# Kernel tuning notes

Measured on AMD Instinct MI355X. Metric: run time of the kernel, lower is better.

Reference implementation:

```python
import jax, jax.numpy as jnp
import numpy as np

B, TQ, TK = 4, 128, 512
DQ = DK = DV = H = 1024


def setup_inputs() -> dict:
    key = jax.random.key(0)
    ks = jax.random.split(key, 7)
    s = 0.05  # keep tanh out of saturation
    return {
        "query": jax.random.normal(ks[0], (B, TQ, DQ), dtype=jnp.float32),
        "key": jax.random.normal(ks[1], (B, TK, DK), dtype=jnp.float32),
        "value": jax.random.normal(ks[2], (B, TK, DV), dtype=jnp.float32),
        "Wq": jax.random.normal(ks[3], (DQ, H), dtype=jnp.float32) * s,
        "bq": jax.random.normal(ks[4], (H,), dtype=jnp.float32) * s,
        "Wk": jax.random.normal(ks[5], (DK, H), dtype=jnp.float32) * s,
        "v": jax.random.normal(ks[6], (H,), dtype=jnp.float32) * s,
    }


def reference(query, key, value, Wq, bq, Wk, v):
    # additive (Bahdanau) attention
    wq = jnp.einsum("bqd,dh->bqh", query, Wq) + bq      # [B,Tq,H]
    uh = jnp.einsum("bkd,dh->bkh", key, Wk)             # [B,Tk,H]
    # broadcast add -> [B,Tq,Tk,H], tanh, project to scalar score
    scores = jnp.einsum("bqkh,h->bqk",
                        jnp.tanh(wq[:, :, None, :] + uh[:, None, :, :]), v)
    attn = jax.nn.softmax(scores, axis=-1)              # [B,Tq,Tk]
    h = jnp.einsum("bqk,bkv->bqv", attn, value)         # [B,Tq,Dv]
    return h, attn
```

## Files before the change

kernel.cpp:

```cpp
#include <hip/hip_runtime.h>
#include <hip/hip_bf16.h>

typedef float f32x4 __attribute__((ext_vector_type(4)));
typedef float f32x2 __attribute__((ext_vector_type(2)));
typedef short s16x8 __attribute__((ext_vector_type(8)));
typedef short s16x4 __attribute__((ext_vector_type(4)));

#define NB  4
#define NTQ 128
#define NTK 512
#define NH  1024
#define ECLAMP 3.0e4f

__device__ __forceinline__ unsigned short f2bf(float x) {
    unsigned u = __builtin_bit_cast(unsigned, x);
    u += 0x7FFFu + ((u >> 16) & 1u);
    return (unsigned short)(u >> 16);
}

#define K2E  2.8853900817779268f

#define GLD16(gp, lp) __builtin_amdgcn_global_load_lds( \
    (const __attribute__((address_space(1))) unsigned int*)(gp), \
    (__attribute__((address_space(3))) unsigned int*)(lp), 16, 0, 0)

__global__ __launch_bounds__(256) void prep_kernel(
    const float* __restrict__ Q, const float* __restrict__ K,
    const float* __restrict__ Wq, const float* __restrict__ Wk,
    const float* __restrict__ value,
    short* __restrict__ Qb, short* __restrict__ Kb,
    short* __restrict__ WqT, short* __restrict__ WkT, short* __restrict__ valT)
{
    const int t = threadIdx.x, bx = blockIdx.x;
    if (bx < 640) {
        const float* src; short* dst; size_t base;
        if (bx < 128) { src = Q; dst = Qb; base = (size_t)bx * 4096; }
        else          { src = K; dst = Kb; base = (size_t)(bx - 128) * 4096; }
        #pragma unroll
        for (int i = 0; i < 4; ++i) {
            const size_t off = base + (size_t)(i * 256 + t) * 4;
            const float4 vv = *(const float4*)(src + off);
            s16x4 o = { (short)f2bf(vv.x), (short)f2bf(vv.y),
                        (short)f2bf(vv.z), (short)f2bf(vv.w) };
            *(s16x4*)(dst + off) = o;
        }
        return;
    }
    __shared__ float tile[64][65];
    const int i = bx - 640;
    const float* src; short* dst; int Cs, Rs, r0, c0;
    if (i < 256)      { src = Wq; dst = WqT; Cs = 1024; Rs = 1024; r0 = (i >> 4) * 64; c0 = (i & 15) * 64; }
    else if (i < 512) { const int j = i - 256; src = Wk; dst = WkT; Cs = 1024; Rs = 1024; r0 = (j >> 4) * 64; c0 = (j & 15) * 64; }
    else {
        const int j = i - 512, b = j >> 7, ti = j & 127;
        src = value + (size_t)b * 512 * 1024; dst = valT + (size_t)b * 1024 * 512;
        Cs = 1024; Rs = 512; r0 = (ti >> 4) * 64; c0 = (ti & 15) * 64;
    }
    {
        const int c = (t & 15) * 4;
        #pragma unroll
        for (int it = 0; it < 4; ++it) {
            const int r = (t >> 4) + it * 16;
            const float4 vv = *(const float4*)(src + (size_t)(r0 + r) * Cs + c0 + c);
            tile[r][c + 0] = vv.x; tile[r][c + 1] = vv.y;
            tile[r][c + 2] = vv.z; tile[r][c + 3] = vv.w;
        }
    }
    __syncthreads();
    {
        const int r = (t & 15) * 4;
        #pragma unroll
        for (int it = 0; it < 4; ++it) {
            const int c = (t >> 4) + it * 16;
            s16x4 o = { (short)f2bf(tile[r + 0][c]), (short)f2bf(tile[r + 1][c]),
                        (short)f2bf(tile[r + 2][c]), (short)f2bf(tile[r + 3][c]) };
            *(s16x4*)(dst + (size_t)(c0 + c) * Rs + r0 + r) = o;
        }
    }
}

__global__ __launch_bounds__(256) void mm_kernel(
    const short* __restrict__ Qb, const short* __restrict__ Kb,
    const short* __restrict__ WqT, const short* __restrict__ WkT,
    const float* __restrict__ bq,
    float* __restrict__ Ea_out, unsigned short* __restrict__ EbT)
{
    __shared__ short ldsA[2][128][64];
    __shared__ short ldsB[2][64][64];
    const int t = threadIdx.x;
    const int bx0 = blockIdx.x;
    const int bx = (bx0 & 7) * 40 + (bx0 >> 3);
    const bool g1 = bx < 64;
    const short *A, *B; int m0, n0;
    if (g1) { A = Qb; B = WqT; m0 = (bx >> 4) * 128; n0 = (bx & 15) * 64; }
    else    { const int i = bx - 64; A = Kb; B = WkT; m0 = (i >> 4) * 128; n0 = (i & 15) * 64; }
    A += (size_t)m0 * 1024; B += (size_t)n0 * 1024;

    f32x4 acc[4][2];
    #pragma unroll
    for (int i = 0; i < 4; ++i)
        #pragma unroll
        for (int j = 0; j < 2; ++j) acc[i][j] = f32x4{0.f, 0.f, 0.f, 0.f};

    const int lane = t & 63, wid = t >> 6;
    const int wr = wid >> 1, wc = wid & 1;
    const int fr = lane & 15, fko = (lane >> 4) * 16;

    #define STAGE_MM(buf, k0) do {                                              \
        _Pragma("unroll")                                                       \
        for (int it = 0; it < 4; ++it) {                                        \
            const int idx = it * 256 + t;                                       \
            const int row = idx >> 3, c16 = idx & 7;                            \
            const int sc = c16 ^ (row & 7);                                     \
            GLD16(A + (size_t)row * 1024 + (k0) + sc * 8,                       \
                  &ldsA[buf][0][0] + idx * 8);                                  \
        }                                                                       \
        _Pragma("unroll")                                                       \
        for (int it = 0; it < 2; ++it) {                                        \
            const int idx = it * 256 + t;                                       \
            const int row = idx >> 3, c16 = idx & 7;                            \
            const int sc = c16 ^ (row & 7);                                     \
            GLD16(B + (size_t)row * 1024 + (k0) + sc * 8,                       \
                  &ldsB[buf][0][0] + idx * 8);                                  \
        }                                                                       \
    } while (0)

    #define COMPUTE_MM(buf) do {                                                \
        _Pragma("unroll")                                                       \
        for (int kk = 0; kk < 2; ++kk) {                                        \
            s16x8 af[4], bfv[2];                                                \
            _Pragma("unroll")                                                   \
            for (int i = 0; i < 4; ++i) {                                       \
                const int rowA = wr * 64 + i * 16 + fr;                         \
                int offA = rowA * 128 + kk * 64 + fko; offA ^= (rowA & 7) << 4; \
                af[i] = *(const s16x8*)((const char*)&ldsA[buf][0][0] + offA);  \
            }                                                                   \
            _Pragma("unroll")                                                   \
            for (int ni = 0; ni < 2; ++ni) {                                    \
                const int rowB = wc * 32 + ni * 16 + fr;                        \
                int offB = rowB * 128 + kk * 64 + fko; offB ^= (rowB & 7) << 4; \
                bfv[ni] = *(const s16x8*)((const char*)&ldsB[buf][0][0] + offB);\
            }                                                                   \
            _Pragma("unroll")                                                   \
            for (int mi = 0; mi < 4; ++mi)                                      \
                _Pragma("unroll")                                               \
                for (int ni = 0; ni < 2; ++ni)                                  \
                    acc[mi][ni] = __builtin_amdgcn_mfma_f32_16x16x32_bf16(      \
                                      af[mi], bfv[ni], acc[mi][ni], 0, 0, 0);   \
        }                                                                       \
    } while (0)

    STAGE_MM(0, 0);
    __syncthreads();
    int cur = 0;
    for (int s = 0; s < 15; ++s) {
        STAGE_MM(cur ^ 1, (s + 1) * 64);
        COMPUTE_MM(cur);
        __syncthreads();
        cur ^= 1;
    }
    COMPUTE_MM(cur);

    const int row0 = (lane >> 4) * 4;
    if (g1) {
        #pragma unroll
        for (int ni = 0; ni < 2; ++ni) {
            const int n = n0 + wc * 32 + ni * 16 + fr;
            const float bias = bq[n];
            #pragma unroll
            for (int mi = 0; mi < 4; ++mi) {
                const int m = m0 + wr * 64 + mi * 16 + row0;
                #pragma unroll
                for (int j = 0; j < 4; ++j)
                    Ea_out[(size_t)(m + j) * 1024 + n] =
                        fminf(__builtin_amdgcn_exp2f(K2E * (acc[mi][ni][j] + bias)), ECLAMP);
            }
        }
    } else {
        #pragma unroll
        for (int mi = 0; mi < 4; ++mi) {
            const int m = m0 + wr * 64 + mi * 16 + row0;
            const int b = m >> 9, kk = m & 511;
            #pragma unroll
            for (int ni = 0; ni < 2; ++ni) {
                const int n = n0 + wc * 32 + ni * 16 + fr;
                s16x4 ev;
                #pragma unroll
                for (int j = 0; j < 4; ++j)
                    ev[j] = (short)f2bf(fminf(__builtin_amdgcn_exp2f(K2E * acc[mi][ni][j]), ECLAMP));
                *(s16x4*)&EbT[((size_t)b * 1024 + n) * 512 + kk] = ev;
            }
        }
    }
    #undef STAGE_MM
    #undef COMPUTE_MM
}

__global__ __launch_bounds__(1024, 4) void scores_softmax(
    const unsigned short* __restrict__ EbT, const float* __restrict__ Ea,
    const float* __restrict__ v,
    float* __restrict__ attn_out, short* __restrict__ attnb)
{
    __shared__ float4 s_eav[1024];
    __shared__ float  s_part[8][2][512];
    __shared__ float  s_red[16];
    const int t = threadIdx.x, bx = blockIdx.x;
    const int b = bx & 3;
    const int q2 = bx >> 2;
    const int bq0 = b * 128 + q2 * 2;
    const int kq = t & 127;
    const int hs = t >> 7;
    const int lane = t & 63, wid = t >> 6;

    s_eav[t] = make_float4(Ea[(size_t)(bq0 + 0) * 1024 + t],
                           Ea[(size_t)(bq0 + 1) * 1024 + t],
                           v[t], 0.f);
    __syncthreads();

    const int h0 = hs * 128;
    const uint2* up = (const uint2*)(EbT + ((size_t)(b * 1024 + h0)) * 512) + kq;
    f32x2 a0lo = {0.f, 0.f}, a0hi = {0.f, 0.f};
    f32x2 a1lo = {0.f, 0.f}, a1hi = {0.f, 0.f};
    const f32x2 one2 = {1.f, 1.f};

    #pragma unroll 2
    for (int hg = 0; hg < 32; ++hg) {
        const int hb = hg * 4;
        const uint2 r0 = up[(size_t)(hb + 0) * 128];
        const uint2 r1 = up[(size_t)(hb + 1) * 128];
        const uint2 r2 = up[(size_t)(hb + 2) * 128];
        const uint2 r3 = up[(size_t)(hb + 3) * 128];
        const float4 ev0 = s_eav[h0 + hb + 0];
        const float4 ev1 = s_eav[h0 + hb + 1];
        const float4 ev2 = s_eav[h0 + hb + 2];
        const float4 ev3 = s_eav[h0 + hb + 3];
        #define UNPK(r) f32x2{__builtin_bit_cast(float, (r) << 16),            \
                              __builtin_bit_cast(float, (r) & 0xFFFF0000u)}
        const f32x2 b0lo = UNPK(r0.x), b0hi = UNPK(r0.y);
        const f32x2 b1lo = UNPK(r1.x), b1hi = UNPK(r1.y);
        const f32x2 b2lo = UNPK(r2.x), b2hi = UNPK(r2.y);
        const f32x2 b3lo = UNPK(r3.x), b3hi = UNPK(r3.y);
        #undef UNPK
        const f32x2 vv0 = {ev0.z, ev0.z}, vv1 = {ev1.z, ev1.z};
        const f32x2 vv2 = {ev2.z, ev2.z}, vv3 = {ev3.z, ev3.z};

        #define GRPPK(accv, EA0, EA1, EA2, EA3, B0, B1, B2, B3) do {            \
            const f32x2 u0 = B0 * EA0 + one2;                                   \
            const f32x2 u1 = B1 * EA1 + one2;                                   \
            const f32x2 u2 = B2 * EA2 + one2;                                   \
            const f32x2 u3 = B3 * EA3 + one2;                                   \
            const f32x2 d01 = u0 * u1, d23 = u2 * u3;                           \
            f32x2 n01 = vv0 * u1; n01 = vv1 * u0 + n01;                         \
            f32x2 n23 = vv2 * u3; n23 = vv3 * u2 + n23;                         \
            f32x2 n = n01 * d23; n = n23 * d01 + n;                             \
            const f32x2 den = d01 * d23;                                        \
            const f32x2 r = {__builtin_amdgcn_rcpf(den.x),                      \
                             __builtin_amdgcn_rcpf(den.y)};                     \
            accv = n * r + accv;                                                \
        } while (0)

        {
            const f32x2 e0 = {ev0.x, ev0.x}, e1 = {ev1.x, ev1.x};
            const f32x2 e2 = {ev2.x, ev2.x}, e3 = {ev3.x, ev3.x};
            GRPPK(a0lo, e0, e1, e2, e3, b0lo, b1lo, b2lo, b3lo);
            GRPPK(a0hi, e0, e1, e2, e3, b0hi, b1hi, b2hi, b3hi);
        }
        {
            const f32x2 e0 = {ev0.y, ev0.y}, e1 = {ev1.y, ev1.y};
            const f32x2 e2 = {ev2.y, ev2.y}, e3 = {ev3.y, ev3.y};
            GRPPK(a1lo, e0, e1, e2, e3, b0lo, b1lo, b2lo, b3lo);
            GRPPK(a1hi, e0, e1, e2, e3, b0hi, b1hi, b2hi, b3hi);
        }
        #undef GRPPK
    }
    *(f32x4*)&s_part[hs][0][kq * 4] = f32x4{a0lo.x, a0lo.y, a0hi.x, a0hi.y};
    *(f32x4*)&s_part[hs][1][kq * 4] = f32x4{a1lo.x, a1lo.y, a1hi.x, a1hi.y};
    __syncthreads();

    const int kk = t & 511, qq = t >> 9;
    float z = 0.f;
    #pragma unroll
    for (int j = 0; j < 8; ++j) z += s_part[j][qq][kk];
    z *= -2.0f;

    float m = z;
    #pragma unroll
    for (int off = 32; off > 0; off >>= 1)
        m = fmaxf(m, __shfl_xor(m, off, 64));
    if (lane == 0) s_red[wid] = m;
    __syncthreads();
    float mx = s_red[qq * 8];
    #pragma unroll
    for (int w = 1; w < 8; ++w) mx = fmaxf(mx, s_red[qq * 8 + w]);
    const float p = __expf(z - mx);
    __syncthreads();

    float sl = p;
    #pragma unroll
    for (int off = 32; off > 0; off >>= 1)
        sl += __shfl_xor(sl, off, 64);
    if (lane == 0) s_red[wid] = sl;
    __syncthreads();
    float s = 0.f;
    #pragma unroll
    for (int w = 0; w < 8; ++w) s += s_red[qq * 8 + w];

    const float a = p * (1.0f / s);
    attn_out[(size_t)(bq0 + qq) * 512 + kk] = a;
    attnb[(size_t)(bq0 + qq) * 512 + kk] = (short)f2bf(a);
}

__global__ __launch_bounds__(256) void pv_gemm(
    const short* __restrict__ attnb, const short* __restrict__ valT,
    float* __restrict__ outh)
{
    __shared__ short ldsA[2][128][64];
    __shared__ short ldsB[2][64][64];
    const int t = threadIdx.x, bx = blockIdx.x;
    const int b = bx >> 4, nt = bx & 15;
    const int n0 = nt * 64;
    const short* A = attnb + (size_t)b * 128 * 512;
    const short* B = valT + (size_t)b * 1024 * 512 + (size_t)n0 * 512;

    f32x4 acc[4][2];
    #pragma unroll
    for (int i = 0; i < 4; ++i)
        #pragma unroll
        for (int j = 0; j < 2; ++j) acc[i][j] = f32x4{0.f, 0.f, 0.f, 0.f};

    const int lane = t & 63, wid = t >> 6;
    const int wr = wid >> 1, wc = wid & 1;
    const int fr = lane & 15, fko = (lane >> 4) * 16;

    #define STAGE_PV(buf, k0) do {                                              \
        _Pragma("unroll")                                                       \
        for (int it = 0; it < 4; ++it) {                                        \
            const int idx = it * 256 + t;                                       \
            const int row = idx >> 3, c16 = idx & 7;                            \
            const int sc = c16 ^ (row & 7);                                     \
            GLD16(A + (size_t)row * 512 + (k0) + sc * 8,                        \
                  &ldsA[buf][0][0] + idx * 8);                                  \
        }                                                                       \
        _Pragma("unroll")                                                       \
        for (int it = 0; it < 2; ++it) {                                        \
            const int idx = it * 256 + t;                                       \
            const int row = idx >> 3, c16 = idx & 7;                            \
            const int sc = c16 ^ (row & 7);                                     \
            GLD16(B + (size_t)row * 512 + (k0) + sc * 8,                        \
                  &ldsB[buf][0][0] + idx * 8);                                  \
        }                                                                       \
    } while (0)

    #define COMPUTE_PV(buf) do {                                                \
        _Pragma("unroll")                                                       \
        for (int kk = 0; kk < 2; ++kk) {                                        \
            s16x8 af[4], bfv[2];                                                \
            _Pragma("unroll")                                                   \
            for (int i = 0; i < 4; ++i) {                                       \
                const int rowA = wr * 64 + i * 16 + fr;                         \
                int offA = rowA * 128 + kk * 64 + fko; offA ^= (rowA & 7) << 4; \
                af[i] = *(const s16x8*)((const char*)&ldsA[buf][0][0] + offA);  \
            }                                                                   \
            _Pragma("unroll")                                                   \
            for (int ni = 0; ni < 2; ++ni) {                                    \
                const int rowB = wc * 32 + ni * 16 + fr;                        \
                int offB = rowB * 128 + kk * 64 + fko; offB ^= (rowB & 7) << 4; \
                bfv[ni] = *(const s16x8*)((const char*)&ldsB[buf][0][0] + offB);\
            }                                                                   \
            _Pragma("unroll")                                                   \
            for (int mi = 0; mi < 4; ++mi)                                      \
                _Pragma("unroll")                                               \
                for (int ni = 0; ni < 2; ++ni)                                  \
                    acc[mi][ni] = __builtin_amdgcn_mfma_f32_16x16x32_bf16(      \
                                      af[mi], bfv[ni], acc[mi][ni], 0, 0, 0);   \
        }                                                                       \
    } while (0)

    STAGE_PV(0, 0);
    __syncthreads();
    int cur = 0;
    for (int s = 0; s < 7; ++s) {
        STAGE_PV(cur ^ 1, (s + 1) * 64);
        COMPUTE_PV(cur);
        __syncthreads();
        cur ^= 1;
    }
    COMPUTE_PV(cur);

    const int row0 = (lane >> 4) * 4;
    #pragma unroll
    for (int ni = 0; ni < 2; ++ni) {
        const int n = n0 + wc * 32 + ni * 16 + fr;
        #pragma unroll
        for (int mi = 0; mi < 4; ++mi) {
            const int m = wr * 64 + mi * 16 + row0;
            #pragma unroll
            for (int j = 0; j < 4; ++j)
                outh[(size_t)(b * 128 + m + j) * 1024 + n] = acc[mi][ni][j];
        }
    }
    #undef STAGE_PV
    #undef COMPUTE_PV
}

extern "C" void kernel_launch(void* const* d_in, const int* in_sizes, int n_in,
                              void* d_out, int out_size, void* d_ws, size_t ws_size,
                              hipStream_t stream)
{
    const float* query = (const float*)d_in[0];
    const float* key   = (const float*)d_in[1];
    const float* value = (const float*)d_in[2];
    const float* Wq    = (const float*)d_in[3];
    const float* bq    = (const float*)d_in[4];
    const float* Wk    = (const float*)d_in[5];
    const float* v     = (const float*)d_in[6];
    float* out = (float*)d_out;

    char* w = (char*)d_ws;
    float*          ws_Ea  = (float*)w;
    unsigned short* ws_EbT = (unsigned short*)(w + (2u << 20));
    short* Qb     = (short*)(w + (6u << 20));
    short* Kb     = (short*)(w + (7u << 20));
    short* WqT    = (short*)(w + (11u << 20));
    short* WkT    = (short*)(w + (13u << 20));
    short* valT   = (short*)(w + (15u << 20));
    short* attnb  = (short*)(w + (19u << 20));

    float* out_h    = out;
    float* out_attn = out + (size_t)NB * NTQ * NH;

    prep_kernel   <<<dim3(1664), dim3(256),  0, stream>>>(query, key, Wq, Wk, value,
                                                          Qb, Kb, WqT, WkT, valT);
    mm_kernel     <<<dim3(320),  dim3(256),  0, stream>>>(Qb, Kb, WqT, WkT, bq, ws_Ea, ws_EbT);
    scores_softmax<<<dim3(256),  dim3(1024), 0, stream>>>(ws_EbT, ws_Ea, v, out_attn, attnb);
    pv_gemm       <<<dim3(64),   dim3(256),  0, stream>>>(attnb, valT, out_h);
}
```

Before: 66.32 us.

## Process one query per scores_softmax block and double the grid size

```diff
diff --git a/kernel.cpp b/kernel.cpp
--- a/kernel.cpp
+++ b/kernel.cpp
@@ -196,31 +196,28 @@
     #undef COMPUTE_MM
 }
 
-__global__ __launch_bounds__(1024, 4) void scores_softmax(
+__global__ __launch_bounds__(1024, 8) void scores_softmax(
     const unsigned short* __restrict__ EbT, const float* __restrict__ Ea,
     const float* __restrict__ v,
     float* __restrict__ attn_out, short* __restrict__ attnb)
 {
-    __shared__ float4 s_eav[1024];
-    __shared__ float  s_part[8][2][512];
+    __shared__ float2 s_eav[1024];
+    __shared__ float  s_part[8][512];
     __shared__ float  s_red[16];
     const int t = threadIdx.x, bx = blockIdx.x;
     const int b = bx & 3;
-    const int q2 = bx >> 2;
-    const int bq0 = b * 128 + q2 * 2;
+    const int q = bx >> 2;
+    const int bq = b * 128 + q;
     const int kq = t & 127;
     const int hs = t >> 7;
     const int lane = t & 63, wid = t >> 6;
 
-    s_eav[t] = make_float4(Ea[(size_t)(bq0 + 0) * 1024 + t],
-                           Ea[(size_t)(bq0 + 1) * 1024 + t],
-                           v[t], 0.f);
+    s_eav[t] = make_float2(Ea[(size_t)bq * 1024 + t], v[t]);
     __syncthreads();
 
     const int h0 = hs * 128;
     const uint2* up = (const uint2*)(EbT + ((size_t)(b * 1024 + h0)) * 512) + kq;
-    f32x2 a0lo = {0.f, 0.f}, a0hi = {0.f, 0.f};
-    f32x2 a1lo = {0.f, 0.f}, a1hi = {0.f, 0.f};
+    f32x2 alo = {0.f, 0.f}, ahi = {0.f, 0.f};
     const f32x2 one2 = {1.f, 1.f};
 
     #pragma unroll 2
@@ -230,10 +227,10 @@
         const uint2 r1 = up[(size_t)(hb + 1) * 128];
         const uint2 r2 = up[(size_t)(hb + 2) * 128];
         const uint2 r3 = up[(size_t)(hb + 3) * 128];
-        const float4 ev0 = s_eav[h0 + hb + 0];
-        const float4 ev1 = s_eav[h0 + hb + 1];
-        const float4 ev2 = s_eav[h0 + hb + 2];
-        const float4 ev3 = s_eav[h0 + hb + 3];
+        const float2 ev0 = s_eav[h0 + hb + 0];
+        const float2 ev1 = s_eav[h0 + hb + 1];
+        const float2 ev2 = s_eav[h0 + hb + 2];
+        const float2 ev3 = s_eav[h0 + hb + 3];
         #define UNPK(r) f32x2{__builtin_bit_cast(float, (r) << 16),            \
                               __builtin_bit_cast(float, (r) & 0xFFFF0000u)}
         const f32x2 b0lo = UNPK(r0.x), b0hi = UNPK(r0.y);
@@ -241,14 +238,16 @@
         const f32x2 b2lo = UNPK(r2.x), b2hi = UNPK(r2.y);
         const f32x2 b3lo = UNPK(r3.x), b3hi = UNPK(r3.y);
         #undef UNPK
-        const f32x2 vv0 = {ev0.z, ev0.z}, vv1 = {ev1.z, ev1.z};
-        const f32x2 vv2 = {ev2.z, ev2.z}, vv3 = {ev3.z, ev3.z};
-
-        #define GRPPK(accv, EA0, EA1, EA2, EA3, B0, B1, B2, B3) do {            \
-            const f32x2 u0 = B0 * EA0 + one2;                                   \
-            const f32x2 u1 = B1 * EA1 + one2;                                   \
-            const f32x2 u2 = B2 * EA2 + one2;                                   \
-            const f32x2 u3 = B3 * EA3 + one2;                                   \
+        const f32x2 e0 = {ev0.x, ev0.x}, e1 = {ev1.x, ev1.x};
+        const f32x2 e2 = {ev2.x, ev2.x}, e3 = {ev3.x, ev3.x};
+        const f32x2 vv0 = {ev0.y, ev0.y}, vv1 = {ev1.y, ev1.y};
+        const f32x2 vv2 = {ev2.y, ev2.y}, vv3 = {ev3.y, ev3.y};
+
+        #define GRPPK(accv, B0, B1, B2, B3) do {                                \
+            const f32x2 u0 = B0 * e0 + one2;                                    \
+            const f32x2 u1 = B1 * e1 + one2;                                    \
+            const f32x2 u2 = B2 * e2 + one2;                                    \
+            const f32x2 u3 = B3 * e3 + one2;                                    \
             const f32x2 d01 = u0 * u1, d23 = u2 * u3;                           \
             f32x2 n01 = vv0 * u1; n01 = vv1 * u0 + n01;                         \
             f32x2 n23 = vv2 * u3; n23 = vv3 * u2 + n23;                         \
@@ -259,28 +258,17 @@
             accv = n * r + accv;                                                \
         } while (0)
 
-        {
-            const f32x2 e0 = {ev0.x, ev0.x}, e1 = {ev1.x, ev1.x};
-            const f32x2 e2 = {ev2.x, ev2.x}, e3 = {ev3.x, ev3.x};
-            GRPPK(a0lo, e0, e1, e2, e3, b0lo, b1lo, b2lo, b3lo);
-            GRPPK(a0hi, e0, e1, e2, e3, b0hi, b1hi, b2hi, b3hi);
-        }
-        {
-            const f32x2 e0 = {ev0.y, ev0.y}, e1 = {ev1.y, ev1.y};
-            const f32x2 e2 = {ev2.y, ev2.y}, e3 = {ev3.y, ev3.y};
-            GRPPK(a1lo, e0, e1, e2, e3, b0lo, b1lo, b2lo, b3lo);
-            GRPPK(a1hi, e0, e1, e2, e3, b0hi, b1hi, b2hi, b3hi);
-        }
+        GRPPK(alo, b0lo, b1lo, b2lo, b3lo);
+        GRPPK(ahi, b0hi, b1hi, b2hi, b3hi);
         #undef GRPPK
     }
-    *(f32x4*)&s_part[hs][0][kq * 4] = f32x4{a0lo.x, a0lo.y, a0hi.x, a0hi.y};
-    *(f32x4*)&s_part[hs][1][kq * 4] = f32x4{a1lo.x, a1lo.y, a1hi.x, a1hi.y};
-    __syncthreads();
-
-    const int kk = t & 511, qq = t >> 9;
+    *(f32x4*)&s_part[hs][kq * 4] = f32x4{alo.x, alo.y, ahi.x, ahi.y};
+    __syncthreads();
+
+    const int kk = t & 511;
     float z = 0.f;
     #pragma unroll
-    for (int j = 0; j < 8; ++j) z += s_part[j][qq][kk];
+    for (int j = 0; j < 8; ++j) z += s_part[j][kk];
     z *= -2.0f;
 
     float m = z;
@@ -289,9 +277,9 @@
         m = fmaxf(m, __shfl_xor(m, off, 64));
     if (lane == 0) s_red[wid] = m;
     __syncthreads();
-    float mx = s_red[qq * 8];
-    #pragma unroll
-    for (int w = 1; w < 8; ++w) mx = fmaxf(mx, s_red[qq * 8 + w]);
+    float mx = s_red[0];
+    #pragma unroll
+    for (int w = 1; w < 8; ++w) mx = fmaxf(mx, s_red[w]);
     const float p = __expf(z - mx);
     __syncthreads();
 
@@ -303,11 +291,13 @@
     __syncthreads();
     float s = 0.f;
     #pragma unroll
-    for (int w = 0; w < 8; ++w) s += s_red[qq * 8 + w];
-
-    const float a = p * (1.0f / s);
-    attn_out[(size_t)(bq0 + qq) * 512 + kk] = a;
-    attnb[(size_t)(bq0 + qq) * 512 + kk] = (short)f2bf(a);
+    for (int w = 0; w < 8; ++w) s += s_red[w];
+
+    if (t < 512) {
+        const float a = p * (1.0f / s);
+        attn_out[(size_t)bq * 512 + kk] = a;
+        attnb[(size_t)bq * 512 + kk] = (short)f2bf(a);
+    }
 }
 
 __global__ __launch_bounds__(256) void pv_gemm(
@@ -432,6 +422,6 @@
     prep_kernel   <<<dim3(1664), dim3(256),  0, stream>>>(query, key, Wq, Wk, value,
                                                           Qb, Kb, WqT, WkT, valT);
     mm_kernel     <<<dim3(320),  dim3(256),  0, stream>>>(Qb, Kb, WqT, WkT, bq, ws_Ea, ws_EbT);
-    scores_softmax<<<dim3(256),  dim3(1024), 0, stream>>>(ws_EbT, ws_Ea, v, out_attn, attnb);
+    scores_softmax<<<dim3(512),  dim3(1024), 0, stream>>>(ws_EbT, ws_Ea, v, out_attn, attnb);
     pv_gemm       <<<dim3(64),   dim3(256),  0, stream>>>(attnb, valT, out_h);
 }
```

After: 72.57 us. +9.4%, slower.
